# Optimization experiments

Hardware: AMD Instinct MI355X
Metric: run time of the kernel (lower is better)

Reference implementation:

```python
import jax, jax.numpy as jnp
import numpy as np

H, W = 256, 512
SCORE_THR = 0.2
NMS_THR = 0.15
TOPK = 4096


def _make_anchors():
    xs = (np.arange(W) + 0.5) * 0.4 - 0.2 * W
    ys = (np.arange(H) + 0.5) * 0.4 - 0.2 * H
    gx, gy = np.meshgrid(xs, ys)            # [H, W]
    anc = np.zeros((H, W, 2, 7), dtype=np.float32)
    anc[..., 0] = gx[..., None]
    anc[..., 1] = gy[..., None]
    anc[..., 2] = -1.0
    anc[..., 3] = 1.56  # h
    anc[..., 4] = 1.6   # w
    anc[..., 5] = 3.9   # l
    anc[..., 0, 6] = 0.0
    anc[..., 1, 6] = np.pi / 2
    return jnp.asarray(anc)


def _make_T(theta, tx, ty, tz):
    c, s = np.cos(theta), np.sin(theta)
    T = np.eye(4, dtype=np.float32)
    T[0, 0], T[0, 1], T[1, 0], T[1, 1] = c, -s, s, c
    T[0, 3], T[1, 3], T[2, 3] = tx, ty, tz
    return jnp.asarray(T)


def setup_inputs() -> dict:
    key = jax.random.key(0)
    k1, k2, k3, k4 = jax.random.split(key, 4)
    return {
        "anchors": _make_anchors(),
        "psm_v": jax.random.normal(k1, (1, 2, H, W), jnp.float32),
        "rm_v": jax.random.normal(k2, (1, 14, H, W), jnp.float32) * 0.1,
        "psm_i": jax.random.normal(k3, (1, 2, H, W), jnp.float32),
        "rm_i": jax.random.normal(k4, (1, 14, H, W), jnp.float32) * 0.1,
        "t_proj": _make_T(0.05, 2.0, -1.0, 0.1),
        "t_ego": _make_T(-0.1, 5.0, 3.0, 0.0),
    }


def delta_to_boxes3d(rm, anchors):
    # rm: [1, 14, H, W] -> [A, 7]; anchors: [H, W, 2, 7] xyzhwlr -> [A, 7]
    d = jnp.transpose(rm[0], (1, 2, 0)).reshape(-1, 7)
    a = anchors.reshape(-1, 7)
    ad = jnp.sqrt(a[:, 4] ** 2 + a[:, 5] ** 2)          # diag of w,l
    xy = d[:, :2] * ad[:, None] + a[:, :2]
    z = d[:, 2] * a[:, 3] + a[:, 2]
    dims = jnp.exp(d[:, 3:6]) * a[:, 3:6]               # h, w, l
    yaw = d[:, 6] + a[:, 6]
    return jnp.concatenate([xy, z[:, None], dims, yaw[:, None]], axis=1)


def boxes_to_corners_3d(b):
    # b: [N, 7] x,y,z,h,w,l,yaw (order 'hwl') -> [N, 8, 3]
    h, w, l, yaw = b[:, 3], b[:, 4], b[:, 5], b[:, 6]
    sx = jnp.array([1, 1, -1, -1, 1, 1, -1, -1], jnp.float32) * 0.5
    sy = jnp.array([1, -1, -1, 1, 1, -1, -1, 1], jnp.float32) * 0.5
    sz = jnp.array([-1, -1, -1, -1, 1, 1, 1, 1], jnp.float32) * 0.5
    x = l[:, None] * sx
    y = w[:, None] * sy
    z = h[:, None] * sz
    c, s = jnp.cos(yaw)[:, None], jnp.sin(yaw)[:, None]
    xr = x * c - y * s + b[:, 0:1]
    yr = x * s + y * c + b[:, 1:2]
    zr = z + b[:, 2:3]
    return jnp.stack([xr, yr, zr], axis=-1)


def project_box3d(corners, T):
    # corners: [N, 8, 3]; T: [4, 4]
    return jnp.einsum('ij,nkj->nki', T[:3, :3], corners) + T[:3, 3]


def corner_to_center(corners):
    # inverse of boxes_to_corners_3d, order 'hwl'
    xyz = corners.mean(axis=1)
    h = corners[:, 4:, 2].mean(axis=1) - corners[:, :4, 2].mean(axis=1)
    dl = corners[:, (0, 1, 4, 5), :2] - corners[:, (3, 2, 7, 6), :2]
    dw = corners[:, (0, 3, 4, 7), :2] - corners[:, (1, 2, 5, 6), :2]
    l = jnp.linalg.norm(dl, axis=-1).mean(axis=1)
    w = jnp.linalg.norm(dw, axis=-1).mean(axis=1)
    d = dl.sum(axis=1)
    yaw = jnp.arctan2(d[:, 1], d[:, 0])
    return jnp.concatenate(
        [xyz, h[:, None], w[:, None], l[:, None], yaw[:, None]], axis=1)


def standup_boxes(corners):
    # [N, 8, 3] -> [N, 4] x1,y1,x2,y2 over BEV
    mn = corners[..., :2].min(axis=1)
    mx = corners[..., :2].max(axis=1)
    return jnp.concatenate([mn, mx], axis=1)


def iou_matrix(b):
    area = (b[:, 2] - b[:, 0]) * (b[:, 3] - b[:, 1])
    lt = jnp.maximum(b[:, None, :2], b[None, :, :2])
    rb = jnp.minimum(b[:, None, 2:], b[None, :, 2:])
    wh = jnp.clip(rb - lt, 0.0)
    inter = wh[..., 0] * wh[..., 1]
    return inter / (area[:, None] + area[None, :] - inter + 1e-6)


def nms_keep(iou, valid, thresh):
    K = iou.shape[0]
    idx = jnp.arange(K)

    def body(i, keep):
        sup = (iou[i] > thresh) & (idx > i) & keep[i]
        return keep & ~sup

    return jax.lax.fori_loop(0, K, body, valid)


def _branch(psm, rm, anchors):
    scores = jax.nn.sigmoid(jnp.transpose(psm[0], (1, 2, 0))).reshape(-1)
    boxes = delta_to_boxes3d(rm, anchors)
    return boxes, scores


def reference(anchors, psm_v, rm_v, psm_i, rm_i, t_proj, t_ego):
    boxes_v, scores_v = _branch(psm_v, rm_v, anchors)
    boxes_i, scores_i = _branch(psm_i, rm_i, anchors)
    # project infra branch boxes into ego frame via corner transform
    corners_i = boxes_to_corners_3d(boxes_i)
    boxes_i = corner_to_center(project_box3d(corners_i, t_proj))
    boxes = jnp.concatenate([boxes_v, boxes_i], axis=0)       # [2A, 7]
    scores = jnp.concatenate([scores_v, scores_i], axis=0)    # [2A]
    # project all to ego space
    proj = project_box3d(boxes_to_corners_3d(boxes), t_ego)   # [2A, 8, 3]
    # static replacement of masked_select: mask + top-K
    masked = jnp.where(scores > SCORE_THR, scores, -1.0)
    top_s, top_i = jax.lax.top_k(masked, TOPK)
    corners_k = proj[top_i]                                    # [K, 8, 3]
    iou = iou_matrix(standup_boxes(corners_k))
    keep = nms_keep(iou, top_s > SCORE_THR, NMS_THR)
    final = top_s * keep.astype(top_s.dtype)
    # pack corners + surviving scores: [K, 25]
    return jnp.concatenate([corners_k.reshape(TOPK, 24), final[:, None]], axis=1)
```

## Files before the change

### kernel.cpp

```cpp
#include <hip/hip_runtime.h>
#include <stdint.h>

typedef unsigned int u32;
typedef unsigned long long u64;

#define HH 256
#define WW 512
#define HW (HH*WW)
#define N2 (2*HW)
#define NT (2*N2)
#define TOPK 4096
#define SCORE_THR 0.2f
#define NMS_THR 0.15f

#define OFF_KEYS   0ull
#define OFF_GHIST  ((size_t)NT*4)
#define OFF_GHIST2 (OFF_GHIST + 4096)
#define OFF_CNT    (OFF_GHIST2 + 4096)
#define OFF_VALIDM (OFF_CNT + 16)
#define OFF_CAND   (OFF_VALIDM + 512)
#define OFF_STAND  OFF_CAND
#define OFF_SELIDX (OFF_CAND + 65536)
#define OFF_SELSC  (OFF_SELIDX + (size_t)TOPK*4)
#define OFF_TDIAG  (OFF_SELSC + (size_t)TOPK*4)
#define ZERO_BYTES (4096 + 4096 + 16)
#define RANK_J 8

#define NMSW 4
#define RPW 16
#define WREG_U64 1088
#define SLOT_U64 (NMSW * WREG_U64)

__device__ __forceinline__ u32 f2ord(float f) {
    u32 b = __float_as_uint(f);
    return (b & 0x80000000u) ? ~b : (b | 0x80000000u);
}

__global__ void __launch_bounds__(1024) k_keys(const float* __restrict__ psm_v,
                                               const float* __restrict__ psm_i,
                                               u32* __restrict__ keys,
                                               u32* __restrict__ ghist) {
    __shared__ u32 lh[1024];
    int t = threadIdx.x;
    lh[t] = 0;
    __syncthreads();
    int n = blockIdx.x * 1024 + t;
    int br = n >> 18;
    int m  = n & (N2 - 1);
    int a  = m & 1;
    int hw = m >> 1;
    const float* psm = br ? psm_i : psm_v;
    float x = psm[a * HW + hw];
    float s = 1.0f / (1.0f + __builtin_expf(-x));
    u32 key = 0u;
    if (s > SCORE_THR) key = f2ord(s);
    keys[n] = key;
    if (key) atomicAdd(&lh[key >> 22], 1u);
    __syncthreads();
    u32 c = lh[t];
    if (c) atomicAdd(&ghist[t], c);
}

__device__ __forceinline__ void pivot1024(const u32* __restrict__ arr, u32 target,
                                          u32* out_bin, u32* out_next, int l) {
    u32 h[16], loc[16];
#pragma unroll
    for (int j = 0; j < 16; ++j) h[j] = arr[l * 16 + j];
    loc[15] = h[15];
#pragma unroll
    for (int j = 14; j >= 0; --j) loc[j] = loc[j + 1] + h[j];
    u32 T = loc[0];
    u32 incl = T;
#pragma unroll
    for (int d = 1; d < 64; d <<= 1) {
        u32 v = __shfl_down(incl, d);
        if (l + d < 64) incl += v;
    }
    u32 E = incl - T;
#pragma unroll
    for (int j = 0; j < 16; ++j) {
        u32 S  = loc[j] + E;
        u32 Sn = (j < 15 ? loc[j + 1] : 0u) + E;
        if (S >= target && Sn < target) {
            *out_bin = (u32)(l * 16 + j);
            *out_next = Sn;
        }
    }
}

__global__ void __launch_bounds__(1024) k_hist2(const u32* __restrict__ ghist,
                                                const u32* __restrict__ keys,
                                                u32* __restrict__ ghist2) {
    __shared__ u32 lh[1024];
    __shared__ u32 b1_sh;
    int tid = threadIdx.x;
    lh[tid] = 0;
    if (tid < 64) {
        u32 bin = 0xFFFFFFFFu, nxt = 0;
        pivot1024(ghist, (u32)TOPK, &bin, &nxt, tid);
        if (bin != 0xFFFFFFFFu) b1_sh = bin;
    }
    __syncthreads();
    u32 b1 = b1_sh;
    int n = blockIdx.x * 1024 + tid;
    u32 key = keys[n];
    if ((key >> 22) == b1) atomicAdd(&lh[(key >> 12) & 1023u], 1u);
    __syncthreads();
    u32 c = lh[tid];
    if (c) atomicAdd(&ghist2[tid], c);
}

__global__ void __launch_bounds__(1024) k_collect(const u32* __restrict__ ghist,
                                                  const u32* __restrict__ ghist2,
                                                  const u32* __restrict__ keys,
                                                  u64* __restrict__ cand,
                                                  u32* __restrict__ cnt) {
    __shared__ u32 b1_sh, t2_sh, b2_sh;
    int tid = threadIdx.x;
    if (tid < 64) {
        u32 bin = 0xFFFFFFFFu, nxt = 0;
        pivot1024(ghist, (u32)TOPK, &bin, &nxt, tid);
        if (bin != 0xFFFFFFFFu) { b1_sh = bin; t2_sh = (u32)TOPK - nxt; }
    }
    __syncthreads();
    if (tid < 64) {
        u32 bin = 0xFFFFFFFFu, nxt = 0;
        pivot1024(ghist2, t2_sh, &bin, &nxt, tid);
        if (bin != 0xFFFFFFFFu) b2_sh = bin;
    }
    __syncthreads();
    u32 thr20 = (b1_sh << 10) | b2_sh;
    int n = blockIdx.x * 1024 + tid;
    u32 key = keys[n];
    if ((key >> 12) >= thr20) {
        u32 pos = atomicAdd(cnt, 1u);
        if (pos < 8192u)
            cand[pos] = ((u64)key << 32) | (u64)(u32)(~(u32)n);
    }
}

__global__ void __launch_bounds__(256) k_rank1(const u64* __restrict__ cand,
                                               const u32* __restrict__ cnt,
                                               u32* __restrict__ partial) {
    __shared__ u64 tile[1024];
    int tid = threadIdx.x;
    int i = blockIdx.x * 256 + tid;
    u32 base = blockIdx.y * 1024u;
    u32 c = *cnt;
    if (c > 8192u) c = 8192u;
    u64 my = (i < (int)c) ? cand[i] : 0ull;
#pragma unroll
    for (int k = 0; k < 4; ++k) {
        u32 idx = base + tid + k * 256;
        tile[tid + k * 256] = (idx < c) ? cand[idx] : 0ull;
    }
    __syncthreads();
    u32 lim = (c > base) ? ((c - base < 1024u) ? (c - base) : 1024u) : 0u;
    u32 r = 0;
#pragma unroll 4
    for (u32 k = 0; k < lim; ++k) r += (tile[k] > my) ? 1u : 0u;
    partial[blockIdx.y * 8192 + i] = r;
}

__global__ void __launch_bounds__(256) k_scatter(const u64* __restrict__ cand,
                                                 const u32* __restrict__ cnt,
                                                 const u32* __restrict__ partial,
                                                 u32* __restrict__ sel_idx) {
    int i = blockIdx.x * 256 + threadIdx.x;
    u32 c = *cnt;
    if (c > 8192u) c = 8192u;
    if (i >= (int)c) return;
    u32 rank = 0;
#pragma unroll
    for (int bj = 0; bj < RANK_J; ++bj) rank += partial[bj * 8192 + i];
    if (rank < (u32)TOPK) {
        u64 my = cand[i];
        sel_idx[rank] = ~((u32)(my & 0xFFFFFFFFull));
    }
}

__device__ __forceinline__ void box_corners(const float b[7], float cx[8], float cy[8], float cz[8]) {
    const float sx[8] = {0.5f,0.5f,-0.5f,-0.5f,0.5f,0.5f,-0.5f,-0.5f};
    const float sy[8] = {0.5f,-0.5f,-0.5f,0.5f,0.5f,-0.5f,-0.5f,0.5f};
    const float sz[8] = {-0.5f,-0.5f,-0.5f,-0.5f,0.5f,0.5f,0.5f,0.5f};
    float c = __builtin_cosf(b[6]), s = __builtin_sinf(b[6]);
#pragma unroll
    for (int k = 0; k < 8; k++) {
        float x = b[5] * sx[k], y = b[4] * sy[k], z = b[3] * sz[k];
        cx[k] = x * c - y * s + b[0];
        cy[k] = x * s + y * c + b[1];
        cz[k] = z + b[2];
    }
}

__device__ __forceinline__ void proj_T(const float* __restrict__ T, float cx[8], float cy[8], float cz[8]) {
#pragma unroll
    for (int k = 0; k < 8; k++) {
        float x = cx[k], y = cy[k], z = cz[k];
        cx[k] = T[0] * x + T[1] * y + T[2]  * z + T[3];
        cy[k] = T[4] * x + T[5] * y + T[6]  * z + T[7];
        cz[k] = T[8] * x + T[9] * y + T[10] * z + T[11];
    }
}

__device__ __forceinline__ void corner_to_center(const float cx[8], const float cy[8], const float cz[8], float b[7]) {
    float mx = 0.f, my = 0.f, mz = 0.f;
#pragma unroll
    for (int k = 0; k < 8; k++) { mx += cx[k]; my += cy[k]; mz += cz[k]; }
    mx *= 0.125f; my *= 0.125f; mz *= 0.125f;
    float htop = (cz[4] + cz[5] + cz[6] + cz[7]) * 0.25f;
    float hbot = (cz[0] + cz[1] + cz[2] + cz[3]) * 0.25f;
    const int lA[4] = {0,1,4,5}, lB[4] = {3,2,7,6};
    const int wA[4] = {0,3,4,7}, wB[4] = {1,2,5,6};
    float l = 0.f, w = 0.f, dx = 0.f, dy = 0.f;
#pragma unroll
    for (int i = 0; i < 4; i++) {
        float ax = cx[lA[i]] - cx[lB[i]];
        float ay = cy[lA[i]] - cy[lB[i]];
        l += __builtin_sqrtf(ax * ax + ay * ay);
        dx += ax; dy += ay;
    }
#pragma unroll
    for (int i = 0; i < 4; i++) {
        float ax = cx[wA[i]] - cx[wB[i]];
        float ay = cy[wA[i]] - cy[wB[i]];
        w += __builtin_sqrtf(ax * ax + ay * ay);
    }
    b[0] = mx; b[1] = my; b[2] = mz;
    b[3] = htop - hbot;
    b[4] = w * 0.25f;
    b[5] = l * 0.25f;
    b[6] = atan2f(dy, dx);
}

__global__ void __launch_bounds__(256) k_boxes(const float* __restrict__ anchors,
                                               const float* __restrict__ psm_v,
                                               const float* __restrict__ psm_i,
                                               const float* __restrict__ rm_v,
                                               const float* __restrict__ rm_i,
                                               const float* __restrict__ tproj,
                                               const float* __restrict__ tego,
                                               const u32* __restrict__ sel_idx,
                                               float* __restrict__ sel_sc,
                                               float* __restrict__ out,
                                               float4* __restrict__ stand,
                                               u64* __restrict__ validm) {
    int k = blockIdx.x * blockDim.x + threadIdx.x;
    if (k >= TOPK) return;
    int n = (int)(sel_idx[k] & (u32)(NT - 1));
    int br = n >> 18;
    int m  = n & (N2 - 1);
    int a  = m & 1;
    int hw = m >> 1;

    const float* psm = br ? psm_i : psm_v;
    float xs = psm[a * HW + hw];
    float s  = 1.0f / (1.0f + __builtin_expf(-xs));
    sel_sc[k] = (s > SCORE_THR) ? s : -1.0f;
    u64 vbits = __ballot(s > SCORE_THR);
    if ((threadIdx.x & 63) == 0) validm[k >> 6] = vbits;

    const float* rm = br ? rm_i : rm_v;
    float d[7];
#pragma unroll
    for (int j = 0; j < 7; j++) d[j] = rm[(a * 7 + j) * HW + hw];
    const float* anc = anchors + (size_t)m * 7;
    float a0 = anc[0], a1 = anc[1], a2 = anc[2], a3 = anc[3], a4 = anc[4], a5 = anc[5], a6 = anc[6];
    float ad = __builtin_sqrtf(a4 * a4 + a5 * a5);
    float b[7];
    b[0] = d[0] * ad + a0;
    b[1] = d[1] * ad + a1;
    b[2] = d[2] * a3 + a2;
    b[3] = __builtin_expf(d[3]) * a3;
    b[4] = __builtin_expf(d[4]) * a4;
    b[5] = __builtin_expf(d[5]) * a5;
    b[6] = d[6] + a6;

    if (br) {
        float cx[8], cy[8], cz[8];
        box_corners(b, cx, cy, cz);
        proj_T(tproj, cx, cy, cz);
        corner_to_center(cx, cy, cz, b);
    }

    float cx[8], cy[8], cz[8];
    box_corners(b, cx, cy, cz);
    proj_T(tego, cx, cy, cz);

    float mnx = cx[0], mny = cy[0], mxx = cx[0], mxy = cy[0];
#pragma unroll
    for (int c = 0; c < 8; c++) {
        out[(size_t)k * 25 + c * 3 + 0] = cx[c];
        out[(size_t)k * 25 + c * 3 + 1] = cy[c];
        out[(size_t)k * 25 + c * 3 + 2] = cz[c];
        mnx = fminf(mnx, cx[c]); mny = fminf(mny, cy[c]);
        mxx = fmaxf(mxx, cx[c]); mxy = fmaxf(mxy, cy[c]);
    }
    stand[k] = make_float4(mnx, mny, mxx, mxy);
}

__global__ void __launch_bounds__(256) k_mask(const float4* __restrict__ stand,
                                              u64* __restrict__ mask) {
    int i = blockIdx.x * 4 + (threadIdx.x >> 6);
    int t = threadIdx.x & 63;
    int w0 = i >> 6;
    float4 bi = stand[i];
    float areai = (bi.z - bi.x) * (bi.w - bi.y);
    u64 myword = 0ull;
    for (int w = w0; w < 64; ++w) {
        int j = w * 64 + t;
        float4 bj = stand[j];
        float areaj = (bj.z - bj.x) * (bj.w - bj.y);
        float ltx = fmaxf(bi.x, bj.x), lty = fmaxf(bi.y, bj.y);
        float rbx = fminf(bi.z, bj.z), rby = fminf(bi.w, bj.w);
        float iw = fmaxf(rbx - ltx, 0.0f), ih = fmaxf(rby - lty, 0.0f);
        float inter = iw * ih;
        float iou = inter / (areai + areaj - inter + 1e-6f);
        bool sup = (iou > NMS_THR) && (j > i);
        u64 bits = __ballot(sup);
        if (t == w) myword = bits;
    }
    mask[(size_t)i * 64 + t] = myword;
}

__global__ void __launch_bounds__(64) k_diag(const float4* __restrict__ stand,
                                             u64* __restrict__ tdiag) {
    __shared__ float4 sb[64];
    int B = blockIdx.x, l = threadIdx.x;
    float4 me = stand[B * 64 + l];
    sb[l] = me;
    __syncthreads();
    float aream = (me.z - me.x) * (me.w - me.y);
    u64 T = 0ull;
    for (int j = 0; j < 64; ++j) {
        float4 bj = sb[j];
        float areaj = (bj.z - bj.x) * (bj.w - bj.y);
        float ltx = fmaxf(bj.x, me.x), lty = fmaxf(bj.y, me.y);
        float rbx = fminf(bj.z, me.z), rby = fminf(bj.w, me.w);
        float iw = fmaxf(rbx - ltx, 0.0f), ih = fmaxf(rby - lty, 0.0f);
        float inter = iw * ih;
        float iou = inter / (areaj + aream - inter + 1e-6f);
        bool sup = (iou > NMS_THR) && (j < l);
        T |= sup ? (1ull << j) : 0ull;
    }
    tdiag[B * 64 + l] = T;
}

__device__ __forceinline__ u64 readlane64(u64 v, int lane) {
    u32 lo = (u32)__builtin_amdgcn_readlane((int)(u32)v, lane);
    u32 hi = (u32)__builtin_amdgcn_readlane((int)(u32)(v >> 32), lane);
    return ((u64)hi << 32) | (u64)lo;
}

__device__ __forceinline__ void nms_stage(const u64* __restrict__ mask,
                                          const u64* __restrict__ tdiag,
                                          int c, int s, int sw, int l,
                                          u64* ring) {
    u64* wb = ring + (size_t)s * SLOT_U64 + (size_t)sw * WREG_U64;
    bool act = (2 * (l & 31) + 1) >= c;
    const u64* gb = mask + (size_t)c * 4096 + (size_t)(sw * RPW) * 64 + (size_t)l * 2;
    if (act) {
#pragma unroll
        for (int k = 0; k < 8; ++k) {
            __builtin_amdgcn_global_load_lds(
                (const __attribute__((address_space(1))) void*)(gb + k * 128),
                (__attribute__((address_space(3))) void*)(wb + k * 128), 16, 0, 0);
        }
    }
    if (l < 32) {
        __builtin_amdgcn_global_load_lds(
            (const __attribute__((address_space(1))) void*)(tdiag + (size_t)c * 64 + (size_t)l * 2),
            (__attribute__((address_space(3))) void*)(wb + 1024), 16, 0, 0);
    }
}

__global__ void __launch_bounds__(NMSW * 64, 1)
k_nms(const u64* __restrict__ mask,
      const u64* __restrict__ tdiag,
      const u64* __restrict__ validm,
      const float* __restrict__ sc,
      float* __restrict__ out) {
    __shared__ u64 ring[3 * SLOT_U64];
    __shared__ u64 sh[2 * NMSW];
    int l  = threadIdx.x & 63;
    int sw = __builtin_amdgcn_readfirstlane((int)(threadIdx.x >> 6));
    u64 remv = 0ull;
    u64 keep = 0ull;
    u64 vreg = validm[l];

    nms_stage(mask, tdiag, 0, 0, sw, l, ring);
    nms_stage(mask, tdiag, 1, 1, sw, l, ring);
    nms_stage(mask, tdiag, 2, 2, sw, l, ring);

    for (int B = 0; B < 64; ++B) {
        int s = B % 3;
        u64* wb = ring + (size_t)s * SLOT_U64 + (size_t)sw * WREG_U64;
        u64 x = readlane64(remv, B);
        if (l == 0) sh[(B & 1) * NMSW + sw] = x;
        __asm__ volatile("" ::: "memory");
        __builtin_amdgcn_s_waitcnt(0xC07F);
        __builtin_amdgcn_s_barrier();
        __asm__ volatile("" ::: "memory");
        __builtin_amdgcn_s_waitcnt(0x4F72);
        __builtin_amdgcn_sched_barrier(0);
        __asm__ volatile("" ::: "memory");
        const volatile u64* sp = sh + (B & 1) * NMSW;
        u64 curw = sp[0] | sp[1] | sp[2] | sp[3];
        u64 Tl = wb[1024 + l];
        u64 row[RPW];
#pragma unroll
        for (int k = 0; k < RPW; ++k) row[k] = wb[(size_t)k * 64 + l];
        u64 vm = readlane64(vreg, B);
        u64 ve = vm & ~curw;
        u64 D = 0ull, P = ve;
        while (D != P) {
            u64 nD = ve & ~__ballot((Tl & P) != 0ull);
            u64 nP = ve & ~__ballot((Tl & nD) != 0ull);
            D = nD; P = nP;
        }
        u64 kb = D;
        keep = (l == B) ? kb : keep;
        u64 kbw = (kb >> (sw * RPW)) & 0xFFFFull;
        u64 p = 0ull;
#pragma unroll
        for (int k = 0; k < RPW; ++k)
            p |= row[k] & (0ull - ((kbw >> k) & 1ull));
        remv |= p;
        if (B + 3 < 64) nms_stage(mask, tdiag, B + 3, s, sw, l, ring);
    }

    for (int k = 0; k < RPW; ++k) {
        int c = sw * RPW + k;
        u64 kc = readlane64(keep, c);
        float s = sc[c * 64 + l];
        out[(size_t)(c * 64 + l) * 25 + 24] = ((kc >> l) & 1ull) ? s : 0.0f;
    }
}

extern "C" void kernel_launch(void* const* d_in, const int* in_sizes, int n_in,
                              void* d_out, int out_size, void* d_ws, size_t ws_size,
                              hipStream_t stream) {
    const float* anchors = (const float*)d_in[0];
    const float* psm_v   = (const float*)d_in[1];
    const float* rm_v    = (const float*)d_in[2];
    const float* psm_i   = (const float*)d_in[3];
    const float* rm_i    = (const float*)d_in[4];
    const float* tproj   = (const float*)d_in[5];
    const float* tego    = (const float*)d_in[6];
    float* out = (float*)d_out;
    char* ws = (char*)d_ws;

    u32*    keys    = (u32*)(ws + OFF_KEYS);
    u64*    mask    = (u64*)(ws + OFF_KEYS);
    u32*    partial = (u32*)(ws + OFF_KEYS);
    u32*    ghist   = (u32*)(ws + OFF_GHIST);
    u32*    ghist2  = (u32*)(ws + OFF_GHIST2);
    u32*    cnt     = (u32*)(ws + OFF_CNT);
    u64*    validm  = (u64*)(ws + OFF_VALIDM);
    u64*    cand    = (u64*)(ws + OFF_CAND);
    float4* stand   = (float4*)(ws + OFF_STAND);
    u32*    sel_idx = (u32*)(ws + OFF_SELIDX);
    float*  sel_sc  = (float*)(ws + OFF_SELSC);
    u64*    tdiag   = (u64*)(ws + OFF_TDIAG);

    hipMemsetAsync(ws + OFF_GHIST, 0, ZERO_BYTES, stream);
    k_keys   <<<NT / 1024, 1024, 0, stream>>>(psm_v, psm_i, keys, ghist);
    k_hist2  <<<NT / 1024, 1024, 0, stream>>>(ghist, keys, ghist2);
    k_collect<<<NT / 1024, 1024, 0, stream>>>(ghist, ghist2, keys, cand, cnt);
    k_rank1  <<<dim3(32, RANK_J), 256, 0, stream>>>(cand, cnt, partial);
    k_scatter<<<32, 256, 0, stream>>>(cand, cnt, partial, sel_idx);
    k_boxes  <<<TOPK / 256, 256, 0, stream>>>(anchors, psm_v, psm_i, rm_v, rm_i,
                                              tproj, tego, sel_idx, sel_sc, out,
                                              stand, validm);
    k_mask   <<<TOPK / 4, 256, 0, stream>>>(stand, mask);
    k_diag   <<<64, 64, 0, stream>>>(stand, tdiag);
    k_nms    <<<1, NMSW * 64, 0, stream>>>(mask, tdiag, validm, sel_sc, out);
}
```

Before: 244.1 us.

## Run NMS sweep on a single wavefront to drop cross-wave barriers

The serial NMS kernel is reduced from four wavefronts to one, so the per-block shared-memory exchange of the removed mask and the s_barrier go away. The one wave now prefetches each full 64-row mask block into LDS with a 3-slot ring and a lookahead of two, using vmcnt waits instead of barriers. Row ORs are skipped for 8-row groups whose keep bits are all zero. In exchange, one wave issues four times the loads per stage with less memory-level parallelism, which may expose load latency on the serial chain.

```diff
diff --git a/kernel.cpp b/kernel.cpp
--- a/kernel.cpp
+++ b/kernel.cpp
@@ -26,10 +26,7 @@
 #define ZERO_BYTES (4096 + 4096 + 16)
 #define RANK_J 8
 
-#define NMSW 4
-#define RPW 16
-#define WREG_U64 1088
-#define SLOT_U64 (NMSW * WREG_U64)
+#define SLOT8 4160
 
 __device__ __forceinline__ u32 f2ord(float f) {
     u32 b = __float_as_uint(f);
@@ -352,64 +349,52 @@
     return ((u64)hi << 32) | (u64)lo;
 }
 
-__device__ __forceinline__ void nms_stage(const u64* __restrict__ mask,
-                                          const u64* __restrict__ tdiag,
-                                          int c, int s, int sw, int l,
-                                          u64* ring) {
-    u64* wb = ring + (size_t)s * SLOT_U64 + (size_t)sw * WREG_U64;
+__device__ __forceinline__ void nms_stage8(const u64* __restrict__ mask,
+                                           const u64* __restrict__ tdiag,
+                                           int c, int l, u64* wb) {
     bool act = (2 * (l & 31) + 1) >= c;
-    const u64* gb = mask + (size_t)c * 4096 + (size_t)(sw * RPW) * 64 + (size_t)l * 2;
+    const u64* gb = mask + (size_t)c * 4096 + (size_t)l * 2;
     if (act) {
 #pragma unroll
-        for (int k = 0; k < 8; ++k) {
+        for (int k = 0; k < 32; ++k) {
             __builtin_amdgcn_global_load_lds(
-                (const __attribute__((address_space(1))) void*)(gb + k * 128),
-                (__attribute__((address_space(3))) void*)(wb + k * 128), 16, 0, 0);
+                (const __attribute__((address_space(1))) void*)(gb + (size_t)k * 128),
+                (__attribute__((address_space(3))) void*)(wb + (size_t)k * 128), 16, 0, 0);
         }
     }
     if (l < 32) {
         __builtin_amdgcn_global_load_lds(
             (const __attribute__((address_space(1))) void*)(tdiag + (size_t)c * 64 + (size_t)l * 2),
-            (__attribute__((address_space(3))) void*)(wb + 1024), 16, 0, 0);
-    }
-}
-
-__global__ void __launch_bounds__(NMSW * 64, 1)
+            (__attribute__((address_space(3))) void*)(wb + 4096), 16, 0, 0);
+    }
+}
+
+__global__ void __launch_bounds__(64, 1)
 k_nms(const u64* __restrict__ mask,
       const u64* __restrict__ tdiag,
       const u64* __restrict__ validm,
       const float* __restrict__ sc,
       float* __restrict__ out) {
-    __shared__ u64 ring[3 * SLOT_U64];
-    __shared__ u64 sh[2 * NMSW];
-    int l  = threadIdx.x & 63;
-    int sw = __builtin_amdgcn_readfirstlane((int)(threadIdx.x >> 6));
+    __shared__ u64 ring[3 * SLOT8];
+    int l = threadIdx.x;
     u64 remv = 0ull;
     u64 keep = 0ull;
     u64 vreg = validm[l];
 
-    nms_stage(mask, tdiag, 0, 0, sw, l, ring);
-    nms_stage(mask, tdiag, 1, 1, sw, l, ring);
-    nms_stage(mask, tdiag, 2, 2, sw, l, ring);
+    nms_stage8(mask, tdiag, 0, l, ring);
+    nms_stage8(mask, tdiag, 1, l, ring + SLOT8);
 
     for (int B = 0; B < 64; ++B) {
         int s = B % 3;
-        u64* wb = ring + (size_t)s * SLOT_U64 + (size_t)sw * WREG_U64;
-        u64 x = readlane64(remv, B);
-        if (l == 0) sh[(B & 1) * NMSW + sw] = x;
-        __asm__ volatile("" ::: "memory");
-        __builtin_amdgcn_s_waitcnt(0xC07F);
-        __builtin_amdgcn_s_barrier();
-        __asm__ volatile("" ::: "memory");
-        __builtin_amdgcn_s_waitcnt(0x4F72);
+        u64* wb = ring + (size_t)s * SLOT8;
+        if (B == 63) __builtin_amdgcn_s_waitcnt(0x0F70);
+        else         __builtin_amdgcn_s_waitcnt(0x8F71);
         __builtin_amdgcn_sched_barrier(0);
         __asm__ volatile("" ::: "memory");
-        const volatile u64* sp = sh + (B & 1) * NMSW;
-        u64 curw = sp[0] | sp[1] | sp[2] | sp[3];
-        u64 Tl = wb[1024 + l];
-        u64 row[RPW];
-#pragma unroll
-        for (int k = 0; k < RPW; ++k) row[k] = wb[(size_t)k * 64 + l];
+        u64 Tl = wb[4096 + l];
+        if (B + 2 < 64)
+            nms_stage8(mask, tdiag, B + 2, l, ring + (size_t)((B + 2) % 3) * SLOT8);
+        u64 curw = readlane64(remv, B);
         u64 vm = readlane64(vreg, B);
         u64 ve = vm & ~curw;
         u64 D = 0ull, P = ve;
@@ -420,17 +405,24 @@
         }
         u64 kb = D;
         keep = (l == B) ? kb : keep;
-        u64 kbw = (kb >> (sw * RPW)) & 0xFFFFull;
+        u32 klo = (u32)__builtin_amdgcn_readfirstlane((int)(u32)kb);
+        u32 khi = (u32)__builtin_amdgcn_readfirstlane((int)(u32)(kb >> 32));
         u64 p = 0ull;
 #pragma unroll
-        for (int k = 0; k < RPW; ++k)
-            p |= row[k] & (0ull - ((kbw >> k) & 1ull));
+        for (int g = 0; g < 8; ++g) {
+            u32 bits = ((g < 4 ? klo : khi) >> ((g & 3) * 8)) & 0xFFu;
+            if (bits) {
+#pragma unroll
+                for (int k = 0; k < 8; ++k) {
+                    u64 row = wb[(size_t)(g * 8 + k) * 64 + l];
+                    p |= row & (0ull - (u64)((bits >> k) & 1u));
+                }
+            }
+        }
         remv |= p;
-        if (B + 3 < 64) nms_stage(mask, tdiag, B + 3, s, sw, l, ring);
-    }
-
-    for (int k = 0; k < RPW; ++k) {
-        int c = sw * RPW + k;
+    }
+
+    for (int c = 0; c < 64; ++c) {
         u64 kc = readlane64(keep, c);
         float s = sc[c * 64 + l];
         out[(size_t)(c * 64 + l) * 25 + 24] = ((kc >> l) & 1ull) ? s : 0.0f;
@@ -474,5 +466,5 @@
                                               stand, validm);
     k_mask   <<<TOPK / 4, 256, 0, stream>>>(stand, mask);
     k_diag   <<<64, 64, 0, stream>>>(stand, tdiag);
-    k_nms    <<<1, NMSW * 64, 0, stream>>>(mask, tdiag, validm, sel_sc, out);
-}
+    k_nms    <<<1, 64, 0, stream>>>(mask, tdiag, validm, sel_sc, out);
+}
```

New measurement: 287.7 us. 17.9% more time.
